# Kernel tuning notes

Measured on AMD Instinct MI355X. Metric: run time of the kernel, lower is better.

The kernel has to match this reference:

```python
import jax, jax.numpy as jnp
import numpy as np

B, T, F, H = 1024, 512, 32, 64
EPS = 1e-3  # keras BatchNormalization default epsilon


def lstm_layer(x, Wx, Uh, b):
    """Keras LSTM with activation=relu, recurrent_activation=sigmoid.
    x: [B,T,Fin]; Wx: [Fin,4H]; Uh: [H,4H]; b: [4H]. Gate order i,f,c,o."""
    xz = jnp.einsum('btf,fg->btg', x, Wx) + b  # precompute input projection
    h0 = jnp.zeros((x.shape[0], Uh.shape[0]), x.dtype)

    def step(carry, xz_t):
        h, c = carry
        z = xz_t + h @ Uh
        i, f, g, o = jnp.split(z, 4, axis=-1)
        i = jax.nn.sigmoid(i)
        f = jax.nn.sigmoid(f)
        o = jax.nn.sigmoid(o)
        c = f * c + i * jax.nn.relu(g)
        h = o * jax.nn.relu(c)
        return (h, c), h

    _, hs = jax.lax.scan(step, (h0, h0), jnp.swapaxes(xz, 0, 1))  # [T,B,H]
    return jnp.swapaxes(hs, 0, 1)  # [B,T,H]


def batchnorm(x, gamma, beta, mean, var):
    # inference-mode BN over last axis (keras default axis=-1, training=False)
    return (x - mean) * (gamma * jax.lax.rsqrt(var + EPS)) + beta


def attention(x, W, ht):
    # score = (X @ W) @ h_t -> [B,T]; softmax over time; c_t = X^T @ alpha
    score = jnp.einsum('btd,de,e->bt', x, W, ht[:, 0])
    alpha = jax.nn.softmax(score, axis=1)
    return jnp.einsum('btd,bt->bd', x, alpha)  # [B,H]


def setup_inputs() -> dict:
    key = jax.random.key(0)
    ks = jax.random.split(key, 32)
    d = {'x': jax.random.normal(ks[0], (B, T, F), jnp.float32)}
    fins = [F, H, H]
    for l in range(3):
        fin = fins[l]
        i = l + 1
        d[f'w{i}'] = jax.random.normal(ks[1 + 9 * l], (fin, 4 * H), jnp.float32) * (1.0 / np.sqrt(fin))
        d[f'u{i}'] = jax.random.normal(ks[2 + 9 * l], (H, 4 * H), jnp.float32) * (1.0 / np.sqrt(H))
        d[f'bi{i}'] = jnp.zeros((4 * H,), jnp.float32)
        d[f'gamma{i}'] = jnp.ones((H,), jnp.float32)
        d[f'beta{i}'] = jnp.zeros((H,), jnp.float32)
        d[f'mean{i}'] = jax.random.normal(ks[3 + 9 * l], (H,), jnp.float32) * 0.1
        d[f'var{i}'] = jnp.ones((H,), jnp.float32) + jax.random.uniform(ks[4 + 9 * l], (H,), jnp.float32) * 0.1
        d[f'attw{i}'] = jax.random.truncated_normal(ks[5 + 9 * l], -2, 2, (H, H), jnp.float32) * 0.5
        d[f'attv{i}'] = jax.random.truncated_normal(ks[6 + 9 * l], -2, 2, (H, 1), jnp.float32) * 0.5
    d['dw'] = jax.random.normal(ks[30], (3 * H, 1), jnp.float32) * (1.0 / np.sqrt(3 * H))
    d['db'] = jnp.zeros((1,), jnp.float32)
    return d


def reference(x, w1, u1, bi1, gamma1, beta1, mean1, var1, attw1, attv1,
              w2, u2, bi2, gamma2, beta2, mean2, var2, attw2, attv2,
              w3, u3, bi3, gamma3, beta3, mean3, var3, attw3, attv3,
              dw, db):
    h = lstm_layer(x, w1, u1, bi1)
    h = batchnorm(h, gamma1, beta1, mean1, var1)
    a1 = attention(h, attw1, attv1)
    h = lstm_layer(h, w2, u2, bi2)
    h = batchnorm(h, gamma2, beta2, mean2, var2)
    a2 = attention(h, attw2, attv2)
    h = lstm_layer(h, w3, u3, bi3)
    h = batchnorm(h, gamma3, beta3, mean3, var3)
    a3 = attention(h, attw3, attv3)
    feat = jnp.concatenate([a1, a2, a3], axis=1)  # [B, 3H]
    return feat @ dw + db  # [B, 1]
```

## Files before the change

kernel.cpp:

```cpp
#include <hip/hip_runtime.h>
#include <math.h>

#define BB 1024
#define TT 512
#define FF 32
#define HH 64
#define GG 256
#define TC 64
#define NCHUNK (TT/TC)
#define MB 16
#define NBLK (BB/MB)
#define HPAD 68
#define EPSBN 1e-3f

typedef __attribute__((ext_vector_type(8))) short bf16x8;
typedef __attribute__((ext_vector_type(4))) float f32x4;
typedef __attribute__((ext_vector_type(4))) int   i32x4;
typedef unsigned short ushort_t;

__global__ void fold1_kernel(const float* __restrict__ gamma, const float* __restrict__ beta,
                             const float* __restrict__ mean, const float* __restrict__ var,
                             const float* __restrict__ attw, const float* __restrict__ attv,
                             float* __restrict__ s_out, float* __restrict__ ab_out,
                             float* __restrict__ wv_out) {
    int d = threadIdx.x;
    float s = gamma[d] * rsqrtf(var[d] + EPSBN);
    float ab = beta[d] - mean[d] * s;
    float wvr = 0.f;
    for (int e = 0; e < HH; ++e) wvr += attw[d * HH + e] * attv[e];
    s_out[d] = s;
    ab_out[d] = ab;
    wv_out[d] = s * wvr;
}

__global__ void fold2_kernel(const float* __restrict__ W, const float* __restrict__ b,
                             const float* __restrict__ s_prev, const float* __restrict__ ab_prev,
                             float* __restrict__ Wp, float* __restrict__ bp) {
    int g = threadIdx.x;
    float bacc = b[g];
    for (int d = 0; d < HH; ++d) {
        float w = W[d * GG + g];
        bacc += ab_prev[d] * w;
        Wp[d * GG + g] = s_prev[d] * w;
    }
    bp[g] = bacc;
}

__global__ void init_kernel(float* st_h, float* st_c, float* st_acc, float* st_m, float* st_d) {
    int i = blockIdx.x * blockDim.x + threadIdx.x;
    int n = 3 * BB * HH;
    if (i < n) { st_h[i] = 0.f; st_c[i] = 0.f; st_acc[i] = 0.f; }
    if (i < 3 * BB) { st_m[i] = -3.0e38f; st_d[i] = 0.f; }
}

__device__ __forceinline__ f32x4 ld4(const float* p) { return *reinterpret_cast<const f32x4*>(p); }
__device__ __forceinline__ void st4(float* p, f32x4 v) { *reinterpret_cast<f32x4*>(p) = v; }
__device__ __forceinline__ int cvtpk(float a, float b) {
    int r; asm("v_cvt_pk_bf16_f32 %0, %1, %2" : "=v"(r) : "v"(a), "v"(b)); return r;
}
__device__ __forceinline__ void mkfrag(f32x4 A, f32x4 B, bf16x8& hi, bf16x8& lo) {
    i32x4 H, L;
    H[0] = cvtpk(A[0], A[1]); H[1] = cvtpk(A[2], A[3]);
    H[2] = cvtpk(B[0], B[1]); H[3] = cvtpk(B[2], B[3]);
    L[0] = cvtpk(A[0] - __int_as_float(H[0] << 16), A[1] - __int_as_float(H[0] & 0xffff0000));
    L[1] = cvtpk(A[2] - __int_as_float(H[1] << 16), A[3] - __int_as_float(H[1] & 0xffff0000));
    L[2] = cvtpk(B[0] - __int_as_float(H[2] << 16), B[1] - __int_as_float(H[2] & 0xffff0000));
    L[3] = cvtpk(B[2] - __int_as_float(H[3] << 16), B[3] - __int_as_float(H[3] & 0xffff0000));
    hi = __builtin_bit_cast(bf16x8, H); lo = __builtin_bit_cast(bf16x8, L);
}
__device__ __forceinline__ float sigm(float x) { return __fdividef(1.f, 1.f + __expf(-x)); }
#define MFMA(a, b, c) c = __builtin_amdgcn_mfma_f32_16x16x32_bf16(a, b, c, 0, 0, 0)

__global__ void prep_frags(const float* __restrict__ M, int KT, ushort_t* __restrict__ outF) {
    int idx = blockIdx.x * 256 + threadIdx.x;
    int tot = 16 * KT * 512;
    if (idx >= tot) return;
    int e = idx & 7, l = (idx >> 3) & 63, f = idx >> 9;
    int kt = f % KT, gw = f / KT;
    int g = gw & 3, w = gw >> 2;
    int r = l & 15, q = l >> 4;
    int k = 32 * kt + 8 * q + e;
    int col = 64 * g + 16 * w + r;
    float v = M[(size_t)k * GG + col];
    int hb = cvtpk(v, v) & 0xffff;
    float hf = __int_as_float(hb << 16);
    float lo = v - hf;
    int lb = cvtpk(lo, lo) & 0xffff;
    outF[(size_t)(f * 2 + 0) * 512 + l * 8 + e] = (ushort_t)hb;
    outF[(size_t)(f * 2 + 1) * 512 + l * 8 + e] = (ushort_t)lb;
}

struct RecFArgs {
    const float* xin[3]; long sB[3]; long sT[3]; int K[3];
    const ushort_t* UF[3]; const ushort_t* WF[3]; const float* bias[3];
    float* Hout[3];
    float* st_h[3]; float* st_c[3]; float* st_acc[3];
    float* st_m[3]; float* st_d[3];
    const float* wv[3]; const float* abv[3]; const float* sbn[3];
    float* a_out[3];
    int last[3]; int first[3];
};

template<int KT>
__device__ __forceinline__ void rec_body(const RecFArgs& A, const int seg, const int b0,
                                         float (*hl)[MB][HPAD]) {
    const int tid = threadIdx.x;
    const int w = tid >> 6;
    const int l = tid & 63;
    const int r = l & 15;
    const int q = l >> 4;
    const int cw = w << 4;
    const int grow = b0 + r;

    const bf16x8* UF = reinterpret_cast<const bf16x8*>(A.UF[seg]);
    const bf16x8* WF = reinterpret_cast<const bf16x8*>(A.WF[seg]);
    bf16x8 UHf[4][2], ULf[4][2], WHf[4][KT], WLf[4][KT];
#pragma unroll
    for (int g = 0; g < 4; ++g) {
#pragma unroll
        for (int kt = 0; kt < 2; ++kt) {
            const int fU = (w * 4 + g) * 2 + kt;
            UHf[g][kt] = UF[(fU * 2 + 0) * 64 + l];
            ULf[g][kt] = UF[(fU * 2 + 1) * 64 + l];
        }
#pragma unroll
        for (int kt = 0; kt < KT; ++kt) {
            const int fW = (w * 4 + g) * KT + kt;
            WHf[g][kt] = WF[(fW * 2 + 0) * 64 + l];
            WLf[g][kt] = WF[(fW * 2 + 1) * 64 + l];
        }
    }
    f32x4 bias4[4];
#pragma unroll
    for (int g = 0; g < 4; ++g) bias4[g] = ld4(A.bias[seg] + 64 * g + cw + 4 * q);
    f32x4 wva = ld4(A.wv[seg] + 8 * q);
    f32x4 wvb = ld4(A.wv[seg] + 8 * q + 4);
    f32x4 wvc = ld4(A.wv[seg] + 32 + 8 * q);
    f32x4 wvd = ld4(A.wv[seg] + 32 + 8 * q + 4);

    f32x4 c4   = ld4(A.st_c[seg]   + (size_t)grow * HH + cw + 4 * q);
    f32x4 h4   = ld4(A.st_h[seg]   + (size_t)grow * HH + cw + 4 * q);
    f32x4 acc4 = ld4(A.st_acc[seg] + (size_t)grow * HH + cw + 4 * q);
    float m_b = A.st_m[seg][grow];
    float d_b = A.st_d[seg][grow];

    st4(&hl[0][r][cw + 4 * q], h4);

    const float* xbase = A.xin[seg] + (size_t)grow * A.sB[seg];
    const long sT = A.sT[seg];

    auto xload = [&](f32x4 (&X)[2 * KT], int t) {
        const float* xp = xbase + (size_t)t * sT + 8 * q;
        X[0] = ld4(xp); X[1] = ld4(xp + 4);
        if constexpr (KT == 2) { X[2] = ld4(xp + 32); X[3] = ld4(xp + 32 + 4); }
    };
    auto seed = [&](f32x4 (&C)[4], f32x4 (&X)[2 * KT]) {
        bf16x8 xh0, xl0, xh1, xl1;
        mkfrag(X[0], X[1], xh0, xl0);
        if constexpr (KT == 2) mkfrag(X[2], X[3], xh1, xl1);
#pragma unroll
        for (int g = 0; g < 4; ++g) {
            C[g] = bias4[g];
            MFMA(WHf[g][0], xh0, C[g]);
            MFMA(WHf[g][0], xl0, C[g]);
            MFMA(WLf[g][0], xh0, C[g]);
            if constexpr (KT == 2) {
                MFMA(WHf[g][1], xh1, C[g]);
                MFMA(WHf[g][1], xl1, C[g]);
                MFMA(WLf[g][1], xh1, C[g]);
            }
        }
    };
    auto attup = [&](f32x4 f0, f32x4 f1, f32x4 f2, f32x4 f3, f32x4 hp4) {
        float sc = 0.f;
#pragma unroll
        for (int i = 0; i < 4; ++i) {
            sc = fmaf(f0[i], wva[i], sc);
            sc = fmaf(f1[i], wvb[i], sc);
            sc = fmaf(f2[i], wvc[i], sc);
            sc = fmaf(f3[i], wvd[i], sc);
        }
        sc += __shfl_xor(sc, 16);
        sc += __shfl_xor(sc, 32);
        float mn = fmaxf(m_b, sc);
        float corr = __expf(m_b - mn);
        float p = __expf(sc - mn);
        d_b = d_b * corr + p;
        acc4 = acc4 * corr + p * hp4;
        m_b = mn;
    };

    f32x4 XA[2 * KT], XB[2 * KT];
    f32x4 Ca[4], Cb[4];
    xload(XA, 0);
    seed(Ca, XA);
    xload(XA, 1);
    xload(XB, 2);
    __syncthreads();

    const bool first = A.first[seg] != 0;
    float* Hob = A.Hout[seg];

    auto STEP = [&](int t, f32x4 (&Cc)[4], f32x4 (&Cn)[4], f32x4 (&X)[2 * KT]) {
        const int pr = t & 1;
        f32x4 f0 = ld4(&hl[pr][r][8 * q]);
        f32x4 f1 = ld4(&hl[pr][r][8 * q + 4]);
        f32x4 f2 = ld4(&hl[pr][r][32 + 8 * q]);
        f32x4 f3 = ld4(&hl[pr][r][32 + 8 * q + 4]);
        f32x4 hp4 = ld4(&hl[pr][r][cw + 4 * q]);
        bf16x8 bh0, bl0, bh1, bl1;
        mkfrag(f0, f1, bh0, bl0);
        mkfrag(f2, f3, bh1, bl1);
#pragma unroll
        for (int g = 0; g < 4; ++g) {
            MFMA(UHf[g][0], bh0, Cc[g]);
            MFMA(UHf[g][0], bl0, Cc[g]);
            MFMA(ULf[g][0], bh0, Cc[g]);
            MFMA(UHf[g][1], bh1, Cc[g]);
            MFMA(UHf[g][1], bl1, Cc[g]);
            MFMA(ULf[g][1], bh1, Cc[g]);
        }
        seed(Cn, X);
        if (!(first && t == 0)) attup(f0, f1, f2, f3, hp4);
        { int tn = t + 3 < TC ? t + 3 : TC - 1; xload(X, tn); }
#pragma unroll
        for (int i = 0; i < 4; ++i) {
            float zi = sigm(Cc[0][i]);
            float zf = sigm(Cc[1][i]);
            float zg = fmaxf(Cc[2][i], 0.f);
            float zo = sigm(Cc[3][i]);
            c4[i] = fmaf(zf, c4[i], zi * zg);
            h4[i] = zo * fmaxf(c4[i], 0.f);
        }
        st4(&hl[pr ^ 1][r][cw + 4 * q], h4);
        if (Hob) st4(Hob + (size_t)grow * (TC * HH) + (size_t)t * HH + cw + 4 * q, h4);
        __syncthreads();
    };

#pragma unroll 1
    for (int it = 0; it < TC / 2; ++it) {
        STEP(2 * it,     Ca, Cb, XA);
        STEP(2 * it + 1, Cb, Ca, XB);
    }

    if (A.last[seg]) {
        f32x4 f0 = ld4(&hl[0][r][8 * q]);
        f32x4 f1 = ld4(&hl[0][r][8 * q + 4]);
        f32x4 f2 = ld4(&hl[0][r][32 + 8 * q]);
        f32x4 f3 = ld4(&hl[0][r][32 + 8 * q + 4]);
        attup(f0, f1, f2, f3, h4);
        f32x4 sb = ld4(A.sbn[seg] + cw + 4 * q);
        f32x4 ab = ld4(A.abv[seg] + cw + 4 * q);
        f32x4 res;
#pragma unroll
        for (int i = 0; i < 4; ++i)
            res[i] = sb[i] * __fdividef(acc4[i], d_b) + ab[i];
        st4(A.a_out[seg] + (size_t)grow * HH + cw + 4 * q, res);
    }
    st4(A.st_c[seg]   + (size_t)grow * HH + cw + 4 * q, c4);
    st4(A.st_h[seg]   + (size_t)grow * HH + cw + 4 * q, h4);
    st4(A.st_acc[seg] + (size_t)grow * HH + cw + 4 * q, acc4);
    if (w == 0 && q == 0) { A.st_m[seg][grow] = m_b; A.st_d[seg][grow] = d_b; }
}

__global__ __launch_bounds__(256, 1) void rec_mfma(RecFArgs A) {
    __shared__ float hl[2][MB][HPAD];
    const int seg = blockIdx.x >> 6;
    const int b0 = (blockIdx.x & (NBLK - 1)) << 4;
    if (A.K[seg] == 32) rec_body<1>(A, seg, b0, hl);
    else                rec_body<2>(A, seg, b0, hl);
}

__global__ void final_kernel(const float* __restrict__ a, const float* __restrict__ dw,
                             const float* __restrict__ db, float* __restrict__ out) {
    int b = blockIdx.x * blockDim.x + threadIdx.x;
    if (b >= BB) return;
    float acc = db[0];
    for (int l = 0; l < 3; ++l)
        for (int j = 0; j < HH; ++j)
            acc += a[(l * BB + b) * HH + j] * dw[l * HH + j];
    out[b] = acc;
}

extern "C" void kernel_launch(void* const* d_in, const int* in_sizes, int n_in,
                              void* d_out, int out_size, void* d_ws, size_t ws_size,
                              hipStream_t stream) {
    (void)in_sizes; (void)n_in; (void)out_size; (void)ws_size;
    const float* x = (const float*)d_in[0];
    const float* w[3]    = {(const float*)d_in[1],  (const float*)d_in[10], (const float*)d_in[19]};
    const float* uu[3]   = {(const float*)d_in[2],  (const float*)d_in[11], (const float*)d_in[20]};
    const float* bi[3]   = {(const float*)d_in[3],  (const float*)d_in[12], (const float*)d_in[21]};
    const float* gam[3]  = {(const float*)d_in[4],  (const float*)d_in[13], (const float*)d_in[22]};
    const float* bet[3]  = {(const float*)d_in[5],  (const float*)d_in[14], (const float*)d_in[23]};
    const float* mea[3]  = {(const float*)d_in[6],  (const float*)d_in[15], (const float*)d_in[24]};
    const float* var[3]  = {(const float*)d_in[7],  (const float*)d_in[16], (const float*)d_in[25]};
    const float* atw[3]  = {(const float*)d_in[8],  (const float*)d_in[17], (const float*)d_in[26]};
    const float* atv[3]  = {(const float*)d_in[9],  (const float*)d_in[18], (const float*)d_in[27]};
    const float* dw = (const float*)d_in[28];
    const float* db = (const float*)d_in[29];

    float* ws = (float*)d_ws;
    size_t off = 0;
    float* Hb[2][2];
    for (int l = 0; l < 2; ++l)
        for (int p = 0; p < 2; ++p) { Hb[l][p] = ws + off; off += (size_t)BB * TC * HH; }
    float* st_h  = ws + off; off += 3 * BB * HH;
    float* st_c  = ws + off; off += 3 * BB * HH;
    float* st_ac = ws + off; off += 3 * BB * HH;
    float* st_m  = ws + off; off += 3 * BB;
    float* st_d  = ws + off; off += 3 * BB;
    float* s_ws  = ws + off; off += 3 * HH;
    float* ab_ws = ws + off; off += 3 * HH;
    float* wv_ws = ws + off; off += 3 * HH;
    float* W2p   = ws + off; off += HH * GG;
    float* W3p   = ws + off; off += HH * GG;
    float* b2p   = ws + off; off += GG;
    float* b3p   = ws + off; off += GG;
    float* a_ws  = ws + off; off += 3 * BB * HH;
    ushort_t* UFb[3]; ushort_t* WFb[3];
    for (int l = 0; l < 3; ++l) { UFb[l] = (ushort_t*)(ws + off); off += 16384; }
    for (int l = 0; l < 3; ++l) { WFb[l] = (ushort_t*)(ws + off); off += 16384; }

    for (int l = 0; l < 3; ++l)
        fold1_kernel<<<1, 64, 0, stream>>>(gam[l], bet[l], mea[l], var[l], atw[l], atv[l],
                                           s_ws + l * HH, ab_ws + l * HH, wv_ws + l * HH);
    fold2_kernel<<<1, 256, 0, stream>>>(w[1], bi[1], s_ws + 0 * HH, ab_ws + 0 * HH, W2p, b2p);
    fold2_kernel<<<1, 256, 0, stream>>>(w[2], bi[2], s_ws + 1 * HH, ab_ws + 1 * HH, W3p, b3p);
    init_kernel<<<(3 * BB * HH + 255) / 256, 256, 0, stream>>>(st_h, st_c, st_ac, st_m, st_d);

    for (int l = 0; l < 3; ++l)
        prep_frags<<<64, 256, 0, stream>>>(uu[l], 2, UFb[l]);
    prep_frags<<<32, 256, 0, stream>>>(w[0], 1, WFb[0]);
    prep_frags<<<64, 256, 0, stream>>>(W2p, 2, WFb[1]);
    prep_frags<<<64, 256, 0, stream>>>(W3p, 2, WFb[2]);

    const float* bl[3] = {bi[0], b2p, b3p};

    for (int s = 0; s <= NCHUNK - 1 + 2; ++s) {
        RecFArgs ra;
        int nseg = 0;
        for (int l = 0; l < 3; ++l) {
            int cpos = s - l;
            if (cpos < 0 || cpos >= NCHUNK) continue;
            if (l == 0) {
                ra.xin[nseg] = x + (size_t)cpos * TC * FF;
                ra.sB[nseg] = (long)TT * FF;
                ra.sT[nseg] = FF;
                ra.K[nseg] = 32;
            } else {
                ra.xin[nseg] = Hb[l - 1][(s & 1) ^ 1];
                ra.sB[nseg] = (long)TC * HH;
                ra.sT[nseg] = HH;
                ra.K[nseg] = 64;
            }
            ra.UF[nseg] = UFb[l]; ra.WF[nseg] = WFb[l]; ra.bias[nseg] = bl[l];
            ra.Hout[nseg] = (l < 2) ? Hb[l][s & 1] : (float*)0;
            ra.st_h[nseg] = st_h + l * BB * HH;
            ra.st_c[nseg] = st_c + l * BB * HH;
            ra.st_acc[nseg] = st_ac + l * BB * HH;
            ra.st_m[nseg] = st_m + l * BB;
            ra.st_d[nseg] = st_d + l * BB;
            ra.wv[nseg]  = wv_ws + l * HH;
            ra.abv[nseg] = ab_ws + l * HH;
            ra.sbn[nseg] = s_ws + l * HH;
            ra.a_out[nseg] = a_ws + l * BB * HH;
            ra.last[nseg]  = (cpos == NCHUNK - 1) ? 1 : 0;
            ra.first[nseg] = (cpos == 0) ? 1 : 0;
            ++nseg;
        }
        if (!nseg) continue;
        rec_mfma<<<nseg * NBLK, 256, 0, stream>>>(ra);
    }
    final_kernel<<<(BB + 255) / 256, 256, 0, stream>>>(a_ws, dw, db, (float*)d_out);
}
```

Before: 800.2 us.

## Drop software-pipelined input seeding; compute full gate GEMM per step with pinned fragments

The recurrent kernel no longer computes the next step's input projection (seed) ahead of time with double-buffered accumulators and a 3-step x prefetch. Each step now computes both the W·x and U·h MFMAs into fresh accumulators, with x prefetched only one step ahead. Weight fragments are held in named scalar variables and pinned with empty asm to keep them in VGPRs. This cuts register pressure and code complexity, but it puts the input-projection MFMAs back on the serial critical path of every timestep.

```diff
diff --git a/kernel.cpp b/kernel.cpp
--- a/kernel.cpp
+++ b/kernel.cpp
@@ -70,6 +70,7 @@
 }
 __device__ __forceinline__ float sigm(float x) { return __fdividef(1.f, 1.f + __expf(-x)); }
 #define MFMA(a, b, c) c = __builtin_amdgcn_mfma_f32_16x16x32_bf16(a, b, c, 0, 0, 0)
+#define PIN(x) asm volatile("" : "+v"(x))
 
 __global__ void prep_frags(const float* __restrict__ M, int KT, ushort_t* __restrict__ outF) {
     int idx = blockIdx.x * 256 + threadIdx.x;
@@ -114,25 +115,32 @@
 
     const bf16x8* UF = reinterpret_cast<const bf16x8*>(A.UF[seg]);
     const bf16x8* WF = reinterpret_cast<const bf16x8*>(A.WF[seg]);
-    bf16x8 UHf[4][2], ULf[4][2], WHf[4][KT], WLf[4][KT];
-#pragma unroll
-    for (int g = 0; g < 4; ++g) {
-#pragma unroll
-        for (int kt = 0; kt < 2; ++kt) {
-            const int fU = (w * 4 + g) * 2 + kt;
-            UHf[g][kt] = UF[(fU * 2 + 0) * 64 + l];
-            ULf[g][kt] = UF[(fU * 2 + 1) * 64 + l];
-        }
-#pragma unroll
-        for (int kt = 0; kt < KT; ++kt) {
-            const int fW = (w * 4 + g) * KT + kt;
-            WHf[g][kt] = WF[(fW * 2 + 0) * 64 + l];
-            WLf[g][kt] = WF[(fW * 2 + 1) * 64 + l];
-        }
-    }
-    f32x4 bias4[4];
-#pragma unroll
-    for (int g = 0; g < 4; ++g) bias4[g] = ld4(A.bias[seg] + 64 * g + cw + 4 * q);
+#define LDU(g,kt,hl_) UF[(((((w<<2)+(g))*2+(kt))*2)+(hl_))*64 + l]
+#define LDW(g,kt,hl_) WF[(((((w<<2)+(g))*KT+(kt))*2)+(hl_))*64 + l]
+    bf16x8 uh00=LDU(0,0,0), uh01=LDU(0,1,0), uh10=LDU(1,0,0), uh11=LDU(1,1,0),
+           uh20=LDU(2,0,0), uh21=LDU(2,1,0), uh30=LDU(3,0,0), uh31=LDU(3,1,0);
+    bf16x8 ul00=LDU(0,0,1), ul01=LDU(0,1,1), ul10=LDU(1,0,1), ul11=LDU(1,1,1),
+           ul20=LDU(2,0,1), ul21=LDU(2,1,1), ul30=LDU(3,0,1), ul31=LDU(3,1,1);
+    bf16x8 wh00=LDW(0,0,0), wh10=LDW(1,0,0), wh20=LDW(2,0,0), wh30=LDW(3,0,0);
+    bf16x8 wl00=LDW(0,0,1), wl10=LDW(1,0,1), wl20=LDW(2,0,1), wl30=LDW(3,0,1);
+    bf16x8 wh01{}, wh11{}, wh21{}, wh31{}, wl01{}, wl11{}, wl21{}, wl31{};
+    if constexpr (KT == 2) {
+        wh01=LDW(0,1,0); wh11=LDW(1,1,0); wh21=LDW(2,1,0); wh31=LDW(3,1,0);
+        wl01=LDW(0,1,1); wl11=LDW(1,1,1); wl21=LDW(2,1,1); wl31=LDW(3,1,1);
+    }
+    PIN(uh00);PIN(uh01);PIN(uh10);PIN(uh11);PIN(uh20);PIN(uh21);PIN(uh30);PIN(uh31);
+    PIN(ul00);PIN(ul01);PIN(ul10);PIN(ul11);PIN(ul20);PIN(ul21);PIN(ul30);PIN(ul31);
+    PIN(wh00);PIN(wh10);PIN(wh20);PIN(wh30);
+    PIN(wl00);PIN(wl10);PIN(wl20);PIN(wl30);
+    if constexpr (KT == 2) {
+        PIN(wh01);PIN(wh11);PIN(wh21);PIN(wh31);
+        PIN(wl01);PIN(wl11);PIN(wl21);PIN(wl31);
+    }
+
+    f32x4 bias40 = ld4(A.bias[seg] +   0 + cw + 4 * q);
+    f32x4 bias41 = ld4(A.bias[seg] +  64 + cw + 4 * q);
+    f32x4 bias42 = ld4(A.bias[seg] + 128 + cw + 4 * q);
+    f32x4 bias43 = ld4(A.bias[seg] + 192 + cw + 4 * q);
     f32x4 wva = ld4(A.wv[seg] + 8 * q);
     f32x4 wvb = ld4(A.wv[seg] + 8 * q + 4);
     f32x4 wvc = ld4(A.wv[seg] + 32 + 8 * q);
@@ -149,29 +157,99 @@
     const float* xbase = A.xin[seg] + (size_t)grow * A.sB[seg];
     const long sT = A.sT[seg];
 
-    auto xload = [&](f32x4 (&X)[2 * KT], int t) {
-        const float* xp = xbase + (size_t)t * sT + 8 * q;
-        X[0] = ld4(xp); X[1] = ld4(xp + 4);
-        if constexpr (KT == 2) { X[2] = ld4(xp + 32); X[3] = ld4(xp + 32 + 4); }
-    };
-    auto seed = [&](f32x4 (&C)[4], f32x4 (&X)[2 * KT]) {
-        bf16x8 xh0, xl0, xh1, xl1;
-        mkfrag(X[0], X[1], xh0, xl0);
-        if constexpr (KT == 2) mkfrag(X[2], X[3], xh1, xl1);
+    f32x4 x0, x1, x2{}, x3{};
+    {
+        const float* xp = xbase + 8 * q;
+        x0 = ld4(xp); x1 = ld4(xp + 4);
+        if constexpr (KT == 2) { x2 = ld4(xp + 32); x3 = ld4(xp + 36); }
+    }
+    __syncthreads();
+
+    const bool first = A.first[seg] != 0;
+    float* Hob = A.Hout[seg];
+
+#pragma unroll 2
+    for (int t = 0; t < TC; ++t) {
+        const int pr = t & 1;
+        const int tn = (t + 1 < TC) ? t + 1 : TC - 1;
+        const float* xp = xbase + (size_t)tn * sT + 8 * q;
+        f32x4 n0 = ld4(xp), n1 = ld4(xp + 4), n2{}, n3{};
+        if constexpr (KT == 2) { n2 = ld4(xp + 32); n3 = ld4(xp + 36); }
+
+        f32x4 f0 = ld4(&hl[pr][r][8 * q]);
+        f32x4 f1 = ld4(&hl[pr][r][8 * q + 4]);
+        f32x4 f2 = ld4(&hl[pr][r][32 + 8 * q]);
+        f32x4 f3 = ld4(&hl[pr][r][32 + 8 * q + 4]);
+        f32x4 hp4 = ld4(&hl[pr][r][cw + 4 * q]);
+
+        bf16x8 bh0, bl0, bh1, bl1, xh0, xl0, xh1, xl1;
+        mkfrag(f0, f1, bh0, bl0);
+        mkfrag(f2, f3, bh1, bl1);
+        mkfrag(x0, x1, xh0, xl0);
+        if constexpr (KT == 2) mkfrag(x2, x3, xh1, xl1);
+
+        f32x4 C0 = bias40;
+        MFMA(wh00, xh0, C0); MFMA(wh00, xl0, C0); MFMA(wl00, xh0, C0);
+        if constexpr (KT == 2) { MFMA(wh01, xh1, C0); MFMA(wh01, xl1, C0); MFMA(wl01, xh1, C0); }
+        MFMA(uh00, bh0, C0); MFMA(uh00, bl0, C0); MFMA(ul00, bh0, C0);
+        MFMA(uh01, bh1, C0); MFMA(uh01, bl1, C0); MFMA(ul01, bh1, C0);
+        f32x4 C1 = bias41;
+        MFMA(wh10, xh0, C1); MFMA(wh10, xl0, C1); MFMA(wl10, xh0, C1);
+        if constexpr (KT == 2) { MFMA(wh11, xh1, C1); MFMA(wh11, xl1, C1); MFMA(wl11, xh1, C1); }
+        MFMA(uh10, bh0, C1); MFMA(uh10, bl0, C1); MFMA(ul10, bh0, C1);
+        MFMA(uh11, bh1, C1); MFMA(uh11, bl1, C1); MFMA(ul11, bh1, C1);
+        f32x4 C2 = bias42;
+        MFMA(wh20, xh0, C2); MFMA(wh20, xl0, C2); MFMA(wl20, xh0, C2);
+        if constexpr (KT == 2) { MFMA(wh21, xh1, C2); MFMA(wh21, xl1, C2); MFMA(wl21, xh1, C2); }
+        MFMA(uh20, bh0, C2); MFMA(uh20, bl0, C2); MFMA(ul20, bh0, C2);
+        MFMA(uh21, bh1, C2); MFMA(uh21, bl1, C2); MFMA(ul21, bh1, C2);
+        f32x4 C3 = bias43;
+        MFMA(wh30, xh0, C3); MFMA(wh30, xl0, C3); MFMA(wl30, xh0, C3);
+        if constexpr (KT == 2) { MFMA(wh31, xh1, C3); MFMA(wh31, xl1, C3); MFMA(wl31, xh1, C3); }
+        MFMA(uh30, bh0, C3); MFMA(uh30, bl0, C3); MFMA(ul30, bh0, C3);
+        MFMA(uh31, bh1, C3); MFMA(uh31, bl1, C3); MFMA(ul31, bh1, C3);
+
+        if (!(first && t == 0)) {
+            float sc = 0.f;
 #pragma unroll
-        for (int g = 0; g < 4; ++g) {
-            C[g] = bias4[g];
-            MFMA(WHf[g][0], xh0, C[g]);
-            MFMA(WHf[g][0], xl0, C[g]);
-            MFMA(WLf[g][0], xh0, C[g]);
-            if constexpr (KT == 2) {
-                MFMA(WHf[g][1], xh1, C[g]);
-                MFMA(WHf[g][1], xl1, C[g]);
-                MFMA(WLf[g][1], xh1, C[g]);
+            for (int i = 0; i < 4; ++i) {
+                sc = fmaf(f0[i], wva[i], sc);
+                sc = fmaf(f1[i], wvb[i], sc);
+                sc = fmaf(f2[i], wvc[i], sc);
+                sc = fmaf(f3[i], wvd[i], sc);
             }
+            sc += __shfl_xor(sc, 16);
+            sc += __shfl_xor(sc, 32);
+            float mn = fmaxf(m_b, sc);
+            float corr = __expf(m_b - mn);
+            float p = __expf(sc - mn);
+            d_b = d_b * corr + p;
+            acc4 = acc4 * corr + p * hp4;
+            m_b = mn;
         }
-    };
-    auto attup = [&](f32x4 f0, f32x4 f1, f32x4 f2, f32x4 f3, f32x4 hp4) {
+
+#pragma unroll
+        for (int i = 0; i < 4; ++i) {
+            float zi = sigm(C0[i]);
+            float zf = sigm(C1[i]);
+            float zg = fmaxf(C2[i], 0.f);
+            float zo = sigm(C3[i]);
+            c4[i] = fmaf(zf, c4[i], zi * zg);
+            h4[i] = zo * fmaxf(c4[i], 0.f);
+        }
+        st4(&hl[pr ^ 1][r][cw + 4 * q], h4);
+        if (Hob) st4(Hob + (size_t)grow * (TC * HH) + (size_t)t * HH + cw + 4 * q, h4);
+
+        x0 = n0; x1 = n1;
+        if constexpr (KT == 2) { x2 = n2; x3 = n3; }
+        __syncthreads();
+    }
+
+    if (A.last[seg]) {
+        f32x4 f0 = ld4(&hl[0][r][8 * q]);
+        f32x4 f1 = ld4(&hl[0][r][8 * q + 4]);
+        f32x4 f2 = ld4(&hl[0][r][32 + 8 * q]);
+        f32x4 f3 = ld4(&hl[0][r][32 + 8 * q + 4]);
         float sc = 0.f;
 #pragma unroll
         for (int i = 0; i < 4; ++i) {
@@ -186,69 +264,8 @@
         float corr = __expf(m_b - mn);
         float p = __expf(sc - mn);
         d_b = d_b * corr + p;
-        acc4 = acc4 * corr + p * hp4;
+        acc4 = acc4 * corr + p * h4;
         m_b = mn;
-    };
-
-    f32x4 XA[2 * KT], XB[2 * KT];
-    f32x4 Ca[4], Cb[4];
-    xload(XA, 0);
-    seed(Ca, XA);
-    xload(XA, 1);
-    xload(XB, 2);
-    __syncthreads();
-
-    const bool first = A.first[seg] != 0;
-    float* Hob = A.Hout[seg];
-
-    auto STEP = [&](int t, f32x4 (&Cc)[4], f32x4 (&Cn)[4], f32x4 (&X)[2 * KT]) {
-        const int pr = t & 1;
-        f32x4 f0 = ld4(&hl[pr][r][8 * q]);
-        f32x4 f1 = ld4(&hl[pr][r][8 * q + 4]);
-        f32x4 f2 = ld4(&hl[pr][r][32 + 8 * q]);
-        f32x4 f3 = ld4(&hl[pr][r][32 + 8 * q + 4]);
-        f32x4 hp4 = ld4(&hl[pr][r][cw + 4 * q]);
-        bf16x8 bh0, bl0, bh1, bl1;
-        mkfrag(f0, f1, bh0, bl0);
-        mkfrag(f2, f3, bh1, bl1);
-#pragma unroll
-        for (int g = 0; g < 4; ++g) {
-            MFMA(UHf[g][0], bh0, Cc[g]);
-            MFMA(UHf[g][0], bl0, Cc[g]);
-            MFMA(ULf[g][0], bh0, Cc[g]);
-            MFMA(UHf[g][1], bh1, Cc[g]);
-            MFMA(UHf[g][1], bl1, Cc[g]);
-            MFMA(ULf[g][1], bh1, Cc[g]);
-        }
-        seed(Cn, X);
-        if (!(first && t == 0)) attup(f0, f1, f2, f3, hp4);
-        { int tn = t + 3 < TC ? t + 3 : TC - 1; xload(X, tn); }
-#pragma unroll
-        for (int i = 0; i < 4; ++i) {
-            float zi = sigm(Cc[0][i]);
-            float zf = sigm(Cc[1][i]);
-            float zg = fmaxf(Cc[2][i], 0.f);
-            float zo = sigm(Cc[3][i]);
-            c4[i] = fmaf(zf, c4[i], zi * zg);
-            h4[i] = zo * fmaxf(c4[i], 0.f);
-        }
-        st4(&hl[pr ^ 1][r][cw + 4 * q], h4);
-        if (Hob) st4(Hob + (size_t)grow * (TC * HH) + (size_t)t * HH + cw + 4 * q, h4);
-        __syncthreads();
-    };
-
-#pragma unroll 1
-    for (int it = 0; it < TC / 2; ++it) {
-        STEP(2 * it,     Ca, Cb, XA);
-        STEP(2 * it + 1, Cb, Ca, XB);
-    }
-
-    if (A.last[seg]) {
-        f32x4 f0 = ld4(&hl[0][r][8 * q]);
-        f32x4 f1 = ld4(&hl[0][r][8 * q + 4]);
-        f32x4 f2 = ld4(&hl[0][r][32 + 8 * q]);
-        f32x4 f3 = ld4(&hl[0][r][32 + 8 * q + 4]);
-        attup(f0, f1, f2, f3, h4);
         f32x4 sb = ld4(A.sbn[seg] + cw + 4 * q);
         f32x4 ab = ld4(A.abv[seg] + cw + 4 * q);
         f32x4 res;
@@ -261,6 +278,8 @@
     st4(A.st_h[seg]   + (size_t)grow * HH + cw + 4 * q, h4);
     st4(A.st_acc[seg] + (size_t)grow * HH + cw + 4 * q, acc4);
     if (w == 0 && q == 0) { A.st_m[seg][grow] = m_b; A.st_d[seg][grow] = d_b; }
+#undef LDU
+#undef LDW
 }
 
 __global__ __launch_bounds__(256, 1) void rec_mfma(RecFArgs A) {
```

After: 789.0 us. About the same (-1.4%).
